# Performance work log

Hardware: AMD Instinct MI355X
Metric: run time of the kernel (lower is better)

The kernel has to match this reference:

```python
import jax, jax.numpy as jnp
import numpy as np

N = 50000
E = 800000


def gcn_conv(x, W, b, src, dst, n_nodes):
    # PyG GCNConv: add self-loops, symmetric deg^-1/2 normalization,
    # out[dst] += norm * (x @ W)[src], then bias.
    h = x @ W  # [N, out]
    src_sl = jnp.concatenate([src, jnp.arange(n_nodes, dtype=src.dtype)])
    dst_sl = jnp.concatenate([dst, jnp.arange(n_nodes, dtype=dst.dtype)])
    deg = jax.ops.segment_sum(jnp.ones_like(dst_sl, dtype=h.dtype), dst_sl,
                              num_segments=n_nodes)  # in-degree incl. self-loop
    dinv = jnp.where(deg > 0, jax.lax.rsqrt(deg), 0.0)
    norm = dinv[src_sl] * dinv[dst_sl]  # [E+N]
    msg = norm[:, None] * h[src_sl]  # gather + scale, [E+N, out]
    out = jax.ops.segment_sum(msg, dst_sl, num_segments=n_nodes)
    return out + b


def setup_inputs() -> dict:
    key = jax.random.key(0)
    ks = jax.random.split(key, 8)
    F, H, O = 128, 128, 64
    x = jax.random.normal(ks[0], (N, F), dtype=jnp.float32)
    edge_index = jax.random.randint(ks[1], (2, E), 0, N, dtype=jnp.int64)
    # Glorot-ish scaled weights
    W1 = jax.random.normal(ks[2], (F, H), dtype=jnp.float32) / np.sqrt(F)
    b1 = jnp.zeros((H,), dtype=jnp.float32)
    W2 = jax.random.normal(ks[3], (H, H), dtype=jnp.float32) / np.sqrt(H)
    b2 = jnp.zeros((H,), dtype=jnp.float32)
    W3 = jax.random.normal(ks[4], (H, O), dtype=jnp.float32) / np.sqrt(H)
    b3 = jnp.zeros((O,), dtype=jnp.float32)
    return {"x": x, "edge_index": edge_index, "W1": W1, "b1": b1,
            "W2": W2, "b2": b2, "W3": W3, "b3": b3}


def reference(x, edge_index, W1, b1, W2, b2, W3, b3):
    src, dst = edge_index[0], edge_index[1]
    h = gcn_conv(x, W1, b1, src, dst, N)
    h = jax.nn.elu(h)
    h = gcn_conv(h, W2, b2, src, dst, N)
    h = jax.nn.elu(h)
    h = gcn_conv(h, W3, b3, src, dst, N)
    return h
```

## Files before the change

### kernel.cpp

```cpp
#include <hip/hip_runtime.h>
#include <hip/hip_fp16.h>
#include <math.h>


#define NFEAT_IN 128
#define SCAN_CHUNK 2048

typedef _Float16 f16x8 __attribute__((ext_vector_type(8)));
typedef float f32x4 __attribute__((ext_vector_type(4)));

__global__ void zero_kernel(int4* __restrict__ p, int n4, int4* __restrict__ eswpad) {
    int i = blockIdx.x * blockDim.x + threadIdx.x;
    int4 z; z.x = z.y = z.z = z.w = 0;
    if (i < n4) p[i] = z;
    if (i < 8) eswpad[i] = z;
}

__global__ __launch_bounds__(256) void countrank_kernel(const int* __restrict__ dst,
                                                        int* __restrict__ cnt,
                                                        int* __restrict__ rank, int E) {
    int i = blockIdx.x * blockDim.x + threadIdx.x;
    int base = i * 4;
    if (base + 4 <= E) {
        int4 d = *(const int4*)&dst[base];
        int4 r;
        r.x = atomicAdd(&cnt[d.x], 1);
        r.y = atomicAdd(&cnt[d.y], 1);
        r.z = atomicAdd(&cnt[d.z], 1);
        r.w = atomicAdd(&cnt[d.w], 1);
        *(int4*)&rank[base] = r;
    } else {
        for (int k = base; k < E; ++k) rank[k] = atomicAdd(&cnt[dst[k]], 1);
    }
}

__global__ __launch_bounds__(256) void reduce_kernel(const int* __restrict__ cnt,
                                                     int* __restrict__ bsum, int n) {
    __shared__ int wtot[4];
    int b = blockIdx.x, t = threadIdx.x;
    int base = b * SCAN_CHUNK + t * 8;
    int s = 0;
    if (base + 8 <= n) {
        int4 a = *(const int4*)&cnt[base];
        int4 c = *(const int4*)&cnt[base + 4];
        s = a.x + a.y + a.z + a.w + c.x + c.y + c.z + c.w;
    } else {
        for (int i = 0; i < 8; ++i) if (base + i < n) s += cnt[base + i];
    }
    int lane = t & 63, wid = t >> 6;
    #pragma unroll
    for (int off = 32; off > 0; off >>= 1) s += __shfl_down(s, off, 64);
    if (lane == 0) wtot[wid] = s;
    __syncthreads();
    if (t == 0) bsum[b] = wtot[0] + wtot[1] + wtot[2] + wtot[3];
}

__global__ __launch_bounds__(256) void scan3_kernel(const int* __restrict__ cnt,
                                                    const int* __restrict__ bsum,
                                                    int* __restrict__ offs,
                                                    float* __restrict__ dinv,
                                                    int n, int nb) {
    __shared__ int wtot[4];
    __shared__ int sbase;
    int b = blockIdx.x, t = threadIdx.x;
    if (t < 64) {
        int val = (t < nb) ? bsum[t] : 0;
        int pre = (t < b) ? val : 0;
        int tot = val;
        #pragma unroll
        for (int off = 32; off > 0; off >>= 1) {
            pre += __shfl_down(pre, off, 64);
            tot += __shfl_down(tot, off, 64);
        }
        if (t == 0) {
            sbase = pre;
            if (b == nb - 1) offs[n] = tot;
        }
    }
    int base = b * SCAN_CHUNK + t * 8;
    int v[8];
    #pragma unroll
    for (int i = 0; i < 8; ++i) v[i] = (base + i < n) ? cnt[base + i] : 0;
    int psum[8], s = 0;
    #pragma unroll
    for (int i = 0; i < 8; ++i) { psum[i] = s; s += v[i]; }
    int lane = t & 63, wid = t >> 6;
    int inc = s;
    #pragma unroll
    for (int off = 1; off < 64; off <<= 1) {
        int tt = __shfl_up(inc, off, 64);
        if (lane >= off) inc += tt;
    }
    if (lane == 63) wtot[wid] = inc;
    __syncthreads();
    int wb = 0;
    for (int w = 0; w < wid; ++w) wb += wtot[w];
    int tbase = sbase + wb + (inc - s);
    #pragma unroll
    for (int i = 0; i < 8; ++i) {
        if (base + i < n) {
            offs[base + i] = tbase + psum[i];
            dinv[base + i] = rsqrtf((float)(v[i] + 1));
        }
    }
}

__global__ __launch_bounds__(256) void fillr_kernel(const int* __restrict__ src,
                                                    const int* __restrict__ dst,
                                                    const int* __restrict__ rank,
                                                    const int* __restrict__ offs,
                                                    const float* __restrict__ dinv,
                                                    int2* __restrict__ esw, int E) {
    int i = blockIdx.x * blockDim.x + threadIdx.x;
    int base = i * 4;
    if (base + 4 <= E) {
        int4 d = *(const int4*)&dst[base];
        int4 r = *(const int4*)&rank[base];
        int4 s = *(const int4*)&src[base];
        int p0 = offs[d.x] + r.x;
        int p1 = offs[d.y] + r.y;
        int p2 = offs[d.z] + r.z;
        int p3 = offs[d.w] + r.w;
        float w0 = dinv[s.x], w1 = dinv[s.y], w2 = dinv[s.z], w3 = dinv[s.w];
        __half2 h0 = __floats2half2_rn(w0, w0);
        __half2 h1 = __floats2half2_rn(w1, w1);
        __half2 h2 = __floats2half2_rn(w2, w2);
        __half2 h3 = __floats2half2_rn(w3, w3);
        int2 e0; e0.x = s.x; e0.y = *(int*)&h0;
        int2 e1; e1.x = s.y; e1.y = *(int*)&h1;
        int2 e2; e2.x = s.z; e2.y = *(int*)&h2;
        int2 e3; e3.x = s.w; e3.y = *(int*)&h3;
        esw[p0] = e0; esw[p1] = e1; esw[p2] = e2; esw[p3] = e3;
    } else {
        for (int k = base; k < E; ++k) {
            int d = dst[k];
            int p = offs[d] + rank[k];
            int s = src[k];
            float w = dinv[s];
            __half2 h = __floats2half2_rn(w, w);
            int2 e; e.x = s; e.y = *(int*)&h;
            esw[p] = e;
        }
    }
}

__global__ __launch_bounds__(256) void convx_kernel(const float* __restrict__ x,
                                                    f16x8* __restrict__ Xf, int nchunk) {
    int i = blockIdx.x * blockDim.x + threadIdx.x;
    if (i >= nchunk) return;
    int m = i >> 4, kc = i & 15;
    float4 a = *(const float4*)&x[(size_t)m * 128 + kc * 8];
    float4 b = *(const float4*)&x[(size_t)m * 128 + kc * 8 + 4];
    f16x8 v;
    v[0] = (_Float16)a.x; v[1] = (_Float16)a.y; v[2] = (_Float16)a.z; v[3] = (_Float16)a.w;
    v[4] = (_Float16)b.x; v[5] = (_Float16)b.y; v[6] = (_Float16)b.z; v[7] = (_Float16)b.w;
    int kt = kc >> 2, sub = kc & 3;
    Xf[(size_t)((m >> 4) * 4 + kt) * 64 + sub * 16 + (m & 15)] = v;
}

__global__ void wfrag_kernel(const float* __restrict__ W1, const float* __restrict__ W2,
                             const float* __restrict__ W3, f16x8* __restrict__ wf1,
                             f16x8* __restrict__ wf2, f16x8* __restrict__ wf3) {
    int b = blockIdx.x;
    const float* W; f16x8* Wf; int NT;
    if (b < 8)       { W = W1; Wf = wf1; NT = 8; }
    else if (b < 16) { W = W2; Wf = wf2; NT = 8; b -= 8; }
    else             { W = W3; Wf = wf3; NT = 4; b -= 16; }
    int c = b * 256 + threadIdx.x;
    if (c >= NT * 256) return;
    int BN = NT * 16;
    int nt = c >> 8;
    int kt = (c >> 6) & 3;
    int l = c & 63;
    int n = nt * 16 + (l & 15);
    int k0 = kt * 32 + (l >> 4) * 8;
    f16x8 v;
    #pragma unroll
    for (int j = 0; j < 8; ++j) v[j] = (_Float16)W[(size_t)(k0 + j) * BN + n];
    Wf[c] = v;
}

template <int NT>
__global__ __launch_bounds__(256) void mgemm_kernel(const f16x8* __restrict__ Xf,
                                                    const f16x8* __restrict__ Wg,
                                                    __half* __restrict__ Y, int mtiles) {
    constexpr int BN = NT * 16;
    __shared__ f16x8 Wf[NT * 4 * 64];
    int t = threadIdx.x;
    #pragma unroll
    for (int i = 0; i < NT; ++i) Wf[t + i * 256] = Wg[t + i * 256];
    __syncthreads();
    int lane = t & 63;
    int mt0 = blockIdx.x * 8 + (t >> 6) * 2;
    #pragma unroll
    for (int it = 0; it < 2; ++it) {
        int mtile = mt0 + it;
        if (mtile >= mtiles) continue;
        const f16x8* xb = Xf + (size_t)mtile * 4 * 64;
        f16x8 bf[4];
        #pragma unroll
        for (int kt = 0; kt < 4; ++kt) bf[kt] = xb[kt * 64 + lane];
        f32x4 acc[NT];
        #pragma unroll
        for (int nt = 0; nt < NT; ++nt) acc[nt] = (f32x4){0.f, 0.f, 0.f, 0.f};
        #pragma unroll
        for (int kt = 0; kt < 4; ++kt) {
            #pragma unroll
            for (int nt = 0; nt < NT; ++nt) {
                f16x8 af = Wf[(nt * 4 + kt) * 64 + lane];
                acc[nt] = __builtin_amdgcn_mfma_f32_16x16x32_f16(af, bf[kt], acc[nt], 0, 0, 0);
            }
        }
        int m = mtile * 16 + (lane & 15);
        int nc0 = (lane >> 4) * 4;
        #pragma unroll
        for (int nt = 0; nt < NT; ++nt) {
            union { __half2 h2[2]; uint2 u; } pk;
            pk.h2[0] = __floats2half2_rn(acc[nt][0], acc[nt][1]);
            pk.h2[1] = __floats2half2_rn(acc[nt][2], acc[nt][3]);
            *(uint2*)&Y[(size_t)m * BN + nt * 16 + nc0] = pk.u;
        }
    }
}

__global__ __launch_bounds__(256) void agg128_kernel(const __half* __restrict__ H,
                                                     const int* __restrict__ offs,
                                                     const int2* __restrict__ esw,
                                                     const float* __restrict__ dinv,
                                                     const float* __restrict__ bias,
                                                     uint4* __restrict__ outf, int n) {
    int lane = threadIdx.x & 63;
    int q = lane >> 4;
    int fl = lane & 15;
    int v = blockIdx.x * 4 + (threadIdx.x >> 6);
    if (v >= n) return;
    float dv = dinv[v];
    int e0 = offs[v], e1 = offs[v + 1];
    int cntE = e1 - e0;
    int nfull = cntE >> 4;
    const char* Hb = (const char*)H + fl * 16;
    __half2 acc[4];
    __half2 zh = __floats2half2_rn(0.f, 0.f);
    acc[0] = zh; acc[1] = zh; acc[2] = zh; acc[3] = zh;
    int e = e0 + q;
    for (int i = 0; i < nfull; ++i, e += 16) {
        #pragma unroll
        for (int j = 0; j < 4; ++j) {
            int2 p = esw[e + 4 * j];
            __half2 w2 = *(__half2*)&p.y;
            uint4 hq = *(const uint4*)(Hb + ((size_t)(unsigned)p.x << 8));
            const __half2* h2 = (const __half2*)&hq;
            acc[0] = __hfma2(h2[0], w2, acc[0]);
            acc[1] = __hfma2(h2[1], w2, acc[1]);
            acc[2] = __hfma2(h2[2], w2, acc[2]);
            acc[3] = __hfma2(h2[3], w2, acc[3]);
        }
    }
    if (cntE & 15) {
        #pragma unroll
        for (int j = 0; j < 4; ++j) {
            int ee = e + 4 * j;
            int2 p = esw[ee];
            int wi = (ee < e1) ? p.y : 0;
            __half2 w2 = *(__half2*)&wi;
            uint4 hq = *(const uint4*)(Hb + ((size_t)(unsigned)p.x << 8));
            const __half2* h2 = (const __half2*)&hq;
            acc[0] = __hfma2(h2[0], w2, acc[0]);
            acc[1] = __hfma2(h2[1], w2, acc[1]);
            acc[2] = __hfma2(h2[2], w2, acc[2]);
            acc[3] = __hfma2(h2[3], w2, acc[3]);
        }
    }
    #pragma unroll
    for (int m = 16; m <= 32; m <<= 1) {
        #pragma unroll
        for (int k = 0; k < 4; ++k) {
            int ai = *(int*)&acc[k];
            int bi = __shfl_xor(ai, m, 64);
            acc[k] = __hadd2(acc[k], *(__half2*)&bi);
        }
    }
    if (q == 0) {
        float a[8];
        #pragma unroll
        for (int k = 0; k < 4; ++k) {
            float2 f = __half22float2(acc[k]);
            a[2 * k] = f.x; a[2 * k + 1] = f.y;
        }
        uint4 hq = *(const uint4*)(Hb + ((size_t)(unsigned)v << 8));
        const _Float16* hp = (const _Float16*)&hq;
        float b[8];
        *(float4*)&b[0] = *(const float4*)&bias[fl * 8];
        *(float4*)&b[4] = *(const float4*)&bias[fl * 8 + 4];
        float r[8];
        #pragma unroll
        for (int k = 0; k < 8; ++k) {
            float t2 = fmaf((float)hp[k], dv, a[k]);
            r[k] = fmaf(dv, t2, b[k]);
            r[k] = r[k] > 0.f ? r[k] : (__expf(r[k]) - 1.f);
        }
        union { __half2 h2[4]; uint4 u; } pk;
        pk.h2[0] = __floats2half2_rn(r[0], r[1]);
        pk.h2[1] = __floats2half2_rn(r[2], r[3]);
        pk.h2[2] = __floats2half2_rn(r[4], r[5]);
        pk.h2[3] = __floats2half2_rn(r[6], r[7]);
        int blockc = (v >> 4) * 4 + (fl >> 2);
        int l2 = (fl & 3) * 16 + (v & 15);
        outf[(size_t)blockc * 64 + l2] = pk.u;
    }
}

__global__ __launch_bounds__(256) void agg64_kernel(const __half* __restrict__ H,
                                                    const int* __restrict__ offs,
                                                    const int2* __restrict__ esw,
                                                    const float* __restrict__ dinv,
                                                    const float* __restrict__ bias,
                                                    float* __restrict__ out, int n) {
    int lane = threadIdx.x & 63;
    int q = lane >> 3;
    int fl = lane & 7;
    int v = blockIdx.x * 4 + (threadIdx.x >> 6);
    if (v >= n) return;
    float dv = dinv[v];
    int e0 = offs[v], e1 = offs[v + 1];
    int cntE = e1 - e0;
    int nfull = cntE >> 4;
    const char* Hb = (const char*)H + fl * 16;
    float a[8];
    #pragma unroll
    for (int k = 0; k < 8; ++k) a[k] = 0.f;
    int e = e0 + q;
    for (int i = 0; i < nfull; ++i, e += 16) {
        #pragma unroll
        for (int j = 0; j < 2; ++j) {
            int2 p = esw[e + 8 * j];
            float w = __low2float(*(const __half2*)&p.y);
            uint4 hq = *(const uint4*)(Hb + ((size_t)(unsigned)p.x << 7));
            const _Float16* hp = (const _Float16*)&hq;
            #pragma unroll
            for (int k = 0; k < 8; ++k) a[k] = fmaf((float)hp[k], w, a[k]);
        }
    }
    if (cntE & 15) {
        #pragma unroll
        for (int j = 0; j < 2; ++j) {
            int ee = e + 8 * j;
            int2 p = esw[ee];
            float w = (ee < e1) ? __low2float(*(const __half2*)&p.y) : 0.f;
            uint4 hq = *(const uint4*)(Hb + ((size_t)(unsigned)p.x << 7));
            const _Float16* hp = (const _Float16*)&hq;
            #pragma unroll
            for (int k = 0; k < 8; ++k) a[k] = fmaf((float)hp[k], w, a[k]);
        }
    }
    #pragma unroll
    for (int m = 8; m <= 32; m <<= 1) {
        #pragma unroll
        for (int k = 0; k < 8; ++k) a[k] += __shfl_xor(a[k], m, 64);
    }
    if (q == 0) {
        uint4 hq = *(const uint4*)(Hb + ((size_t)(unsigned)v << 7));
        const _Float16* hp = (const _Float16*)&hq;
        float b[8];
        *(float4*)&b[0] = *(const float4*)&bias[fl * 8];
        *(float4*)&b[4] = *(const float4*)&bias[fl * 8 + 4];
        float r[8];
        #pragma unroll
        for (int k = 0; k < 8; ++k) {
            float t2 = fmaf((float)hp[k], dv, a[k]);
            r[k] = fmaf(dv, t2, b[k]);
        }
        float4 o0, o1;
        o0.x = r[0]; o0.y = r[1]; o0.z = r[2]; o0.w = r[3];
        o1.x = r[4]; o1.y = r[5]; o1.z = r[6]; o1.w = r[7];
        *(float4*)&out[(size_t)v * 64 + fl * 8] = o0;
        *(float4*)&out[(size_t)v * 64 + fl * 8 + 4] = o1;
    }
}

static inline size_t alignup(size_t x) { return (x + 255) & ~(size_t)255; }

extern "C" void kernel_launch(void* const* d_in, const int* in_sizes, int n_in,
                              void* d_out, int out_size, void* d_ws, size_t ws_size,
                              hipStream_t stream) {
    const float* x  = (const float*)d_in[0];
    const int*   ei = (const int*)d_in[1];
    const float* W1 = (const float*)d_in[2];
    const float* b1 = (const float*)d_in[3];
    const float* W2 = (const float*)d_in[4];
    const float* b2 = (const float*)d_in[5];
    const float* W3 = (const float*)d_in[6];
    const float* b3 = (const float*)d_in[7];
    float* out = (float*)d_out;

    const int N = in_sizes[0] / NFEAT_IN;
    const int E = in_sizes[1] / 2;
    const int* src = ei;
    const int* dst = ei + E;

    char* w = (char*)d_ws;
    int* cnt  = (int*)w;  w += alignup((size_t)N * sizeof(int));
    int* rank = (int*)w;  w += alignup((size_t)E * sizeof(int));
    int* offs = (int*)w;  w += alignup((size_t)(N + 1) * sizeof(int));
    float* dinv = (float*)w; w += alignup((size_t)N * sizeof(float));
    int* bsum = (int*)w;  w += alignup((size_t)64 * sizeof(int));
    int2* esw = (int2*)w; w += alignup((size_t)(E + 16) * sizeof(int2));
    __half* fA = (__half*)w; w += alignup((size_t)N * 128 * sizeof(__half));
    __half* hB = (__half*)w; w += alignup((size_t)N * 128 * sizeof(__half));
    f16x8* wf1 = (f16x8*)w; w += alignup((size_t)2048 * sizeof(f16x8));
    f16x8* wf2 = (f16x8*)w; w += alignup((size_t)2048 * sizeof(f16x8));
    f16x8* wf3 = (f16x8*)w; w += alignup((size_t)1024 * sizeof(f16x8));

    const int nb = (N + SCAN_CHUNK - 1) / SCAN_CHUNK;
    const int mtiles = N / 16;
    const int egrid = (E / 4 + 255) / 256;

    zero_kernel<<<(N / 4 + 255) / 256, 256, 0, stream>>>((int4*)cnt, N / 4, (int4*)(esw + E));
    countrank_kernel<<<egrid, 256, 0, stream>>>(dst, cnt, rank, E);
    reduce_kernel<<<nb, 256, 0, stream>>>(cnt, bsum, N);
    scan3_kernel<<<nb, 256, 0, stream>>>(cnt, bsum, offs, dinv, N, nb);
    fillr_kernel<<<egrid, 256, 0, stream>>>(src, dst, rank, offs, dinv, esw, E);

    wfrag_kernel<<<20, 256, 0, stream>>>(W1, W2, W3, wf1, wf2, wf3);
    convx_kernel<<<(N * 16 + 255) / 256, 256, 0, stream>>>(x, (f16x8*)fA, N * 16);

    int gemm_grid = (mtiles + 7) / 8;
    int agg_grid = (N + 3) / 4;

    mgemm_kernel<8><<<gemm_grid, 256, 0, stream>>>((const f16x8*)fA, wf1, hB, mtiles);
    agg128_kernel<<<agg_grid, 256, 0, stream>>>(hB, offs, esw, dinv, b1, (uint4*)fA, N);
    mgemm_kernel<8><<<gemm_grid, 256, 0, stream>>>((const f16x8*)fA, wf2, hB, mtiles);
    agg128_kernel<<<agg_grid, 256, 0, stream>>>(hB, offs, esw, dinv, b2, (uint4*)fA, N);
    mgemm_kernel<4><<<gemm_grid, 256, 0, stream>>>((const f16x8*)fA, wf3, hB, mtiles);
    agg64_kernel<<<agg_grid, 256, 0, stream>>>(hB, offs, esw, dinv, b3, out, N);
}
```

Baseline: 195.6 us.

## Replace global-atomic CSR build with sharded LDS histogram counting sort

Replaces the global-atomic count/rank pass and rank-based fill with a two-pass sharded counting sort. Each block keeps a shared-memory histogram for one of 8 destination shards over one edge chunk, and a per-node prefix over block histograms gives per-block offsets. The scatter then uses LDS atomics instead of global ones. Every block reads its whole edge chunk once per shard, so edge reads grow eightfold, and a 64x-per-shard histogram array is added to the workspace.

```diff
diff --git a/kernel.cpp b/kernel.cpp
--- a/kernel.cpp
+++ b/kernel.cpp
@@ -5,33 +5,64 @@
 
 #define NFEAT_IN 128
 #define SCAN_CHUNK 2048
+#define NSHARD 8
+#define BPS 64
+#define SHARD_MAX 6272
 
 typedef _Float16 f16x8 __attribute__((ext_vector_type(8)));
 typedef float f32x4 __attribute__((ext_vector_type(4)));
 
-__global__ void zero_kernel(int4* __restrict__ p, int n4, int4* __restrict__ eswpad) {
-    int i = blockIdx.x * blockDim.x + threadIdx.x;
-    int4 z; z.x = z.y = z.z = z.w = 0;
-    if (i < n4) p[i] = z;
-    if (i < 8) eswpad[i] = z;
-}
-
-__global__ __launch_bounds__(256) void countrank_kernel(const int* __restrict__ dst,
-                                                        int* __restrict__ cnt,
-                                                        int* __restrict__ rank, int E) {
-    int i = blockIdx.x * blockDim.x + threadIdx.x;
-    int base = i * 4;
-    if (base + 4 <= E) {
-        int4 d = *(const int4*)&dst[base];
-        int4 r;
-        r.x = atomicAdd(&cnt[d.x], 1);
-        r.y = atomicAdd(&cnt[d.y], 1);
-        r.z = atomicAdd(&cnt[d.z], 1);
-        r.w = atomicAdd(&cnt[d.w], 1);
-        *(int4*)&rank[base] = r;
-    } else {
-        for (int k = base; k < E; ++k) rank[k] = atomicAdd(&cnt[dst[k]], 1);
-    }
+__global__ void zeropad_kernel(int4* __restrict__ eswpad) {
+    if (threadIdx.x < 8) { int4 z; z.x = z.y = z.z = z.w = 0; eswpad[threadIdx.x] = z; }
+}
+
+__global__ __launch_bounds__(256) void histA_kernel(const int* __restrict__ dst,
+                                                    int* __restrict__ histG,
+                                                    int E, int chunk, int shard_sz) {
+    int s = blockIdx.x & (NSHARD - 1);
+    int b = blockIdx.x >> 3;
+    int lo = s * shard_sz;
+    __shared__ int h[SHARD_MAX];
+    for (int j = threadIdx.x; j < shard_sz; j += 256) h[j] = 0;
+    __syncthreads();
+    int i0 = b * chunk;
+    int i1 = min(i0 + chunk, E);
+    for (int i = i0 + threadIdx.x * 4; i < i1; i += 1024) {
+        if (i + 4 <= i1) {
+            int4 d = *(const int4*)&dst[i];
+            if ((unsigned)(d.x - lo) < (unsigned)shard_sz) atomicAdd(&h[d.x - lo], 1);
+            if ((unsigned)(d.y - lo) < (unsigned)shard_sz) atomicAdd(&h[d.y - lo], 1);
+            if ((unsigned)(d.z - lo) < (unsigned)shard_sz) atomicAdd(&h[d.z - lo], 1);
+            if ((unsigned)(d.w - lo) < (unsigned)shard_sz) atomicAdd(&h[d.w - lo], 1);
+        } else {
+            for (int k = i; k < i1; ++k) {
+                int d = dst[k];
+                if ((unsigned)(d - lo) < (unsigned)shard_sz) atomicAdd(&h[d - lo], 1);
+            }
+        }
+    }
+    __syncthreads();
+    int gbase = (s * BPS + b) * shard_sz;
+    for (int j = threadIdx.x; j < shard_sz; j += 256) histG[gbase + j] = h[j];
+}
+
+__global__ __launch_bounds__(256) void histprefix_kernel(int* __restrict__ histG,
+                                                         int* __restrict__ cnt,
+                                                         int n, int shard_sz) {
+    int j = blockIdx.x * 256 + threadIdx.x;
+    if (j >= n) return;
+    int s = j / shard_sz;
+    int local = j - s * shard_sz;
+    int base = (s * BPS) * shard_sz + local;
+    int run = 0;
+    #pragma unroll 4
+    for (int b = 0; b < BPS; ++b) {
+        int idx = base + b * shard_sz;
+        int t = histG[idx];
+        histG[idx] = run;
+        run += t;
+    }
+    cnt[j] = run;
 }
 
 __global__ __launch_bounds__(256) void reduce_kernel(const int* __restrict__ cnt,
@@ -105,41 +136,54 @@
     }
 }
 
-__global__ __launch_bounds__(256) void fillr_kernel(const int* __restrict__ src,
+__global__ __launch_bounds__(256) void scatC_kernel(const int* __restrict__ src,
                                                     const int* __restrict__ dst,
-                                                    const int* __restrict__ rank,
+                                                    const int* __restrict__ histG,
                                                     const int* __restrict__ offs,
                                                     const float* __restrict__ dinv,
-                                                    int2* __restrict__ esw, int E) {
-    int i = blockIdx.x * blockDim.x + threadIdx.x;
-    int base = i * 4;
-    if (base + 4 <= E) {
-        int4 d = *(const int4*)&dst[base];
-        int4 r = *(const int4*)&rank[base];
-        int4 s = *(const int4*)&src[base];
-        int p0 = offs[d.x] + r.x;
-        int p1 = offs[d.y] + r.y;
-        int p2 = offs[d.z] + r.z;
-        int p3 = offs[d.w] + r.w;
-        float w0 = dinv[s.x], w1 = dinv[s.y], w2 = dinv[s.z], w3 = dinv[s.w];
-        __half2 h0 = __floats2half2_rn(w0, w0);
-        __half2 h1 = __floats2half2_rn(w1, w1);
-        __half2 h2 = __floats2half2_rn(w2, w2);
-        __half2 h3 = __floats2half2_rn(w3, w3);
-        int2 e0; e0.x = s.x; e0.y = *(int*)&h0;
-        int2 e1; e1.x = s.y; e1.y = *(int*)&h1;
-        int2 e2; e2.x = s.z; e2.y = *(int*)&h2;
-        int2 e3; e3.x = s.w; e3.y = *(int*)&h3;
-        esw[p0] = e0; esw[p1] = e1; esw[p2] = e2; esw[p3] = e3;
-    } else {
-        for (int k = base; k < E; ++k) {
-            int d = dst[k];
-            int p = offs[d] + rank[k];
-            int s = src[k];
-            float w = dinv[s];
-            __half2 h = __floats2half2_rn(w, w);
-            int2 e; e.x = s; e.y = *(int*)&h;
-            esw[p] = e;
+                                                    int2* __restrict__ esw,
+                                                    int E, int chunk, int shard_sz, int n) {
+    int s = blockIdx.x & (NSHARD - 1);
+    int b = blockIdx.x >> 3;
+    int lo = s * shard_sz;
+    __shared__ int cur[SHARD_MAX];
+    int gbase = (s * BPS + b) * shard_sz;
+    for (int j = threadIdx.x; j < shard_sz; j += 256) {
+        int g = lo + j;
+        int o = (g < n) ? offs[g] : 0;
+        cur[j] = o + histG[gbase + j];
+    }
+    __syncthreads();
+    int i0 = b * chunk;
+    int i1 = min(i0 + chunk, E);
+    for (int i = i0 + threadIdx.x * 4; i < i1; i += 1024) {
+        if (i + 4 <= i1) {
+            int4 d = *(const int4*)&dst[i];
+            int4 sv = *(const int4*)&src[i];
+            #pragma unroll
+            for (int k = 0; k < 4; ++k) {
+                int dd = (&d.x)[k];
+                if ((unsigned)(dd - lo) < (unsigned)shard_sz) {
+                    int ss = (&sv.x)[k];
+                    int p = atomicAdd(&cur[dd - lo], 1);
+                    float w = dinv[ss];
+                    __half2 h = __floats2half2_rn(w, w);
+                    int2 e; e.x = ss; e.y = *(int*)&h;
+                    esw[p] = e;
+                }
+            }
+        } else {
+            for (int k = i; k < i1; ++k) {
+                int dd = dst[k];
+                if ((unsigned)(dd - lo) < (unsigned)shard_sz) {
+                    int ss = src[k];
+                    int p = atomicAdd(&cur[dd - lo], 1);
+                    float w = dinv[ss];
+                    __half2 h = __floats2half2_rn(w, w);
+                    int2 e; e.x = ss; e.y = *(int*)&h;
+                    esw[p] = e;
+                }
+            }
         }
     }
 }
@@ -398,28 +442,31 @@
     const int* src = ei;
     const int* dst = ei + E;
 
+    const int shard_sz = (N + NSHARD - 1) / NSHARD;
+    const int chunk = (((E + BPS - 1) / BPS) + 3) & ~3;
+    const int nb = (N + SCAN_CHUNK - 1) / SCAN_CHUNK;
+    const int mtiles = N / 16;
+
     char* w = (char*)d_ws;
     int* cnt  = (int*)w;  w += alignup((size_t)N * sizeof(int));
-    int* rank = (int*)w;  w += alignup((size_t)E * sizeof(int));
     int* offs = (int*)w;  w += alignup((size_t)(N + 1) * sizeof(int));
     float* dinv = (float*)w; w += alignup((size_t)N * sizeof(float));
     int* bsum = (int*)w;  w += alignup((size_t)64 * sizeof(int));
     int2* esw = (int2*)w; w += alignup((size_t)(E + 16) * sizeof(int2));
+    int* histG = (int*)w; w += alignup((size_t)NSHARD * BPS * shard_sz * sizeof(int));
     __half* fA = (__half*)w; w += alignup((size_t)N * 128 * sizeof(__half));
     __half* hB = (__half*)w; w += alignup((size_t)N * 128 * sizeof(__half));
     f16x8* wf1 = (f16x8*)w; w += alignup((size_t)2048 * sizeof(f16x8));
     f16x8* wf2 = (f16x8*)w; w += alignup((size_t)2048 * sizeof(f16x8));
     f16x8* wf3 = (f16x8*)w; w += alignup((size_t)1024 * sizeof(f16x8));
 
-    const int nb = (N + SCAN_CHUNK - 1) / SCAN_CHUNK;
-    const int mtiles = N / 16;
-    const int egrid = (E / 4 + 255) / 256;
-
-    zero_kernel<<<(N / 4 + 255) / 256, 256, 0, stream>>>((int4*)cnt, N / 4, (int4*)(esw + E));
-    countrank_kernel<<<egrid, 256, 0, stream>>>(dst, cnt, rank, E);
+    zeropad_kernel<<<1, 64, 0, stream>>>((int4*)(esw + E));
+    histA_kernel<<<NSHARD * BPS, 256, 0, stream>>>(dst, histG, E, chunk, shard_sz);
+    histprefix_kernel<<<(N + 255) / 256, 256, 0, stream>>>(histG, cnt, N, shard_sz);
     reduce_kernel<<<nb, 256, 0, stream>>>(cnt, bsum, N);
     scan3_kernel<<<nb, 256, 0, stream>>>(cnt, bsum, offs, dinv, N, nb);
-    fillr_kernel<<<egrid, 256, 0, stream>>>(src, dst, rank, offs, dinv, esw, E);
+    scatC_kernel<<<NSHARD * BPS, 256, 0, stream>>>(src, dst, histG, offs, dinv, esw,
+                                                   E, chunk, shard_sz, N);
 
     wfrag_kernel<<<20, 256, 0, stream>>>(W1, W2, W3, wf1, wf2, wf3);
     convx_kernel<<<(N * 16 + 255) / 256, 256, 0, stream>>>(x, (f16x8*)fA, N * 16);
```

After: 200.4 us. 1.02x slower.
